# Optimization experiments

Hardware: AMD Instinct MI355X
Metric: run time of the kernel (lower is better)

The kernel has to match this reference:

```python
import jax, jax.numpy as jnp
import numpy as np

N_NODES = 10000
N_EDGES = 320000
NODE_F = 64
EDGE_F = 32
H = 256
L = 6
HEADS = 8
OUT = H // HEADS
N_GRAPHS = 16
NEG_SLOPE = 0.2  # PyG GATConv leaky_relu slope


def setup_inputs() -> dict:
    key = jax.random.key(0)
    ks = jax.random.split(key, 32)
    s = 0.05
    f32 = jnp.float32
    inp = {}
    inp["x"] = jax.random.normal(ks[0], (N_NODES, NODE_F), f32)
    inp["edge_index"] = jax.random.randint(ks[1], (2, N_EDGES), 0, N_NODES)
    inp["edge_attr"] = jax.random.normal(ks[2], (N_EDGES, EDGE_F), f32)
    inp["batch"] = jnp.sort(jax.random.randint(ks[3], (N_NODES,), 0, N_GRAPHS))
    # embeddings
    inp["node_w"] = jax.random.normal(ks[4], (H, NODE_F), f32) * s
    inp["node_b"] = jnp.zeros((H,), f32)
    inp["edge_emb_w"] = jax.random.normal(ks[5], (H, EDGE_F), f32) * s
    inp["edge_emb_b"] = jnp.zeros((H,), f32)
    # stacked GATConv params (shared lin for src/dst since in_channels is int)
    inp["lin_w"] = jax.random.normal(ks[6], (L, H, H), f32) * s
    inp["att_src"] = jax.random.normal(ks[7], (L, HEADS, OUT), f32) * s
    inp["att_dst"] = jax.random.normal(ks[8], (L, HEADS, OUT), f32) * s
    inp["att_edge"] = jax.random.normal(ks[9], (L, HEADS, OUT), f32) * s
    inp["lin_edge_w"] = jax.random.normal(ks[10], (L, H, H), f32) * s
    inp["conv_b"] = jnp.zeros((L, H), f32)
    inp["ln_g"] = jnp.ones((L, H), f32)
    inp["ln_b"] = jnp.zeros((L, H), f32)
    # MLP heads: Linear(2H->H), Linear(H->H/2), Linear(H/2->3)
    inp["pw1"] = jax.random.normal(ks[11], (H, 2 * H), f32) * s
    inp["pb1"] = jnp.zeros((H,), f32)
    inp["pw2"] = jax.random.normal(ks[12], (H // 2, H), f32) * s
    inp["pb2"] = jnp.zeros((H // 2,), f32)
    inp["pw3"] = jax.random.normal(ks[13], (3, H // 2), f32) * s
    inp["pb3"] = jnp.zeros((3,), f32)
    inp["mw1"] = jax.random.normal(ks[14], (H, 2 * H), f32) * s
    inp["mb1"] = jnp.zeros((H,), f32)
    inp["mw2"] = jax.random.normal(ks[15], (H // 2, H), f32) * s
    inp["mb2"] = jnp.zeros((H // 2,), f32)
    inp["mw3"] = jax.random.normal(ks[16], (3, H // 2), f32) * s
    inp["mb3"] = jnp.zeros((3,), f32)
    return inp


def _ln(x, g, b):
    mu = jnp.mean(x, -1, keepdims=True)
    var = jnp.mean(jnp.square(x - mu), -1, keepdims=True)
    return g * (x - mu) * jax.lax.rsqrt(var + 1e-5) + b


def _mlp(z, w1, b1, w2, b2, w3, b3):
    h = jax.nn.gelu(z @ w1.T + b1, approximate=False)
    h = jax.nn.gelu(h @ w2.T + b2, approximate=False)
    return jax.nn.sigmoid(h @ w3.T + b3)


def _gnn_forward(x, edge_attr, src, dst, batch,
                 node_w, node_b, edge_emb_w, edge_emb_b,
                 lin_w, att_src, att_dst, att_edge, lin_edge_w, conv_b,
                 ln_g, ln_b,
                 pw1, pb1, pw2, pb2, pw3, pb3,
                 mw1, mb1, mw2, mb2, mw3, mb3):
    h = x @ node_w.T + node_b                       # [N, H]
    ea = edge_attr @ edge_emb_w.T + edge_emb_b      # [E, H]
    # PyG add_self_loops(fill_value='mean'): loop attr = mean of incoming edge attrs
    cnt = jax.ops.segment_sum(jnp.ones((N_EDGES,), h.dtype), dst, N_NODES)
    loop_attr = jax.ops.segment_sum(ea, dst, N_NODES) / jnp.maximum(cnt, 1.0)[:, None]
    ea_full = jnp.concatenate([ea, loop_attr], 0)   # [E+N, H]
    loops = jnp.arange(N_NODES, dtype=src.dtype)
    src_f = jnp.concatenate([src, loops])
    dst_f = jnp.concatenate([dst, loops])
    for i in range(L):
        x_in = h
        xw = (h @ lin_w[i].T).reshape(N_NODES, HEADS, OUT)
        eap = (ea_full @ lin_edge_w[i].T).reshape(-1, HEADS, OUT)
        a_src = jnp.sum(xw * att_src[i], -1)        # [N, heads]
        a_dst = jnp.sum(xw * att_dst[i], -1)
        alpha = a_src[src_f] + a_dst[dst_f] + jnp.sum(eap * att_edge[i], -1)  # [E+N, heads]
        alpha = jnp.where(alpha > 0, alpha, NEG_SLOPE * alpha)
        amax = jax.ops.segment_max(alpha, dst_f, N_NODES)
        e = jnp.exp(alpha - amax[dst_f])
        denom = jax.ops.segment_sum(e, dst_f, N_NODES)
        w = e / (denom[dst_f] + 1e-16)
        msg = xw[src_f] * w[:, :, None]             # [E+N, heads, out]
        hi = jax.ops.segment_sum(msg, dst_f, N_NODES).reshape(N_NODES, H) + conv_b[i]
        hi = jax.nn.gelu(_ln(hi, ln_g[i], ln_b[i]), approximate=False)
        h = hi + x_in if i > 0 else hi
    sums = jax.ops.segment_sum(h, batch, N_GRAPHS)  # [G, H]
    ncnt = jax.ops.segment_sum(jnp.ones((N_NODES,), h.dtype), batch, N_GRAPHS)
    mean = sums / jnp.maximum(ncnt, 1.0)[:, None]
    xg = jnp.concatenate([mean, sums], 1)           # [G, 2H]
    params = _mlp(xg, pw1, pb1, pw2, pb2, pw3, pb3)
    metrics = _mlp(xg, mw1, mb1, mw2, mb2, mw3, mb3)
    return params, metrics


def reference(x, edge_index, edge_attr, batch,
              node_w, node_b, edge_emb_w, edge_emb_b,
              lin_w, att_src, att_dst, att_edge, lin_edge_w, conv_b,
              ln_g, ln_b,
              pw1, pb1, pw2, pb2, pw3, pb3,
              mw1, mb1, mw2, mb2, mw3, mb3):
    return _gnn_forward(x, edge_attr, edge_index[0], edge_index[1], batch,
                        node_w, node_b, edge_emb_w, edge_emb_b,
                        lin_w, att_src, att_dst, att_edge, lin_edge_w, conv_b,
                        ln_g, ln_b,
                        pw1, pb1, pw2, pb2, pw3, pb3,
                        mw1, mb1, mw2, mb2, mw3, mb3)
```

## Files before the change

### kernel.cpp

```cpp
#include <hip/hip_runtime.h>
#include <math.h>

#define NN 10000
#define NE 320000
#define NODE_F 64
#define EDGE_F 32
#define HDIM 256
#define HEADS 8
#define LAYERS 6
#define NG 16
#define NPB 2
#define NOUT 48
#define LOG2E 1.4426950408889634f

typedef __attribute__((ext_vector_type(8))) short short8;
typedef __attribute__((ext_vector_type(4))) float float4v;
typedef __attribute__((ext_vector_type(2))) float floatx2;

__global__ void count_kernel(const int* __restrict__ dst, int* __restrict__ cnt) {
    int e = blockIdx.x * 256 + threadIdx.x;
    if (e < NE) atomicAdd(&cnt[dst[e]], 1);
}

__global__ void scan_kernel(const int* __restrict__ cnt, int* __restrict__ row_ptr,
                            int* __restrict__ pos) {
    __shared__ int part[1024];
    int t = threadIdx.x;
    const int chunk = (NN + 1023) / 1024;
    int lo = t * chunk, hi = min(NN, lo + chunk);
    int s = 0;
    for (int i = lo; i < hi; ++i) s += cnt[i];
    part[t] = s;
    __syncthreads();
    for (int off = 1; off < 1024; off <<= 1) {
        int v = (t >= off) ? part[t - off] : 0;
        __syncthreads();
        part[t] += v;
        __syncthreads();
    }
    int base = (t == 0) ? 0 : part[t - 1];
    for (int i = lo; i < hi; ++i) {
        row_ptr[i] = base;
        pos[i] = base;
        base += cnt[i];
    }
    if (t == 1023) row_ptr[NN] = part[1023];
}

__device__ __forceinline__ ushort f2bf(float f) {
    union { float f; unsigned u; } v; v.f = f;
    unsigned u = v.u;
    return (ushort)((u + 0x7fffu + ((u >> 16) & 1u)) >> 16);
}
__device__ __forceinline__ float bf2f(ushort b) {
    union { unsigned u; float f; } v; v.u = ((unsigned)b) << 16; return v.f;
}

__global__ void scatter_kernel(const int* __restrict__ src, const int* __restrict__ dst,
                               const float* __restrict__ edge_attr,
                               int* __restrict__ pos, int* __restrict__ csr_src,
                               ushort* __restrict__ ea_bf) {
    int e = blockIdx.x * 256 + threadIdx.x;
    if (e >= NE) return;
    int d = dst[e];
    int idx = atomicAdd(&pos[d], 1);
    csr_src[idx] = src[e];
    const float4* p = (const float4*)(edge_attr + (size_t)e * EDGE_F);
    uint4* q = (uint4*)(ea_bf + (size_t)idx * EDGE_F);
    #pragma unroll
    for (int i = 0; i < 4; ++i) {
        float4 v0 = p[i * 2], v1 = p[i * 2 + 1];
        uint4 pk;
        pk.x = (unsigned)f2bf(v0.x) | ((unsigned)f2bf(v0.y) << 16);
        pk.y = (unsigned)f2bf(v0.z) | ((unsigned)f2bf(v0.w) << 16);
        pk.z = (unsigned)f2bf(v1.x) | ((unsigned)f2bf(v1.y) << 16);
        pk.w = (unsigned)f2bf(v1.z) | ((unsigned)f2bf(v1.w) << 16);
        q[i] = pk;
    }
}

__global__ __launch_bounds__(256) void prep_kernel(const float* __restrict__ att_edge,
                                                   const float* __restrict__ lin_edge_w,
                                                   const float* __restrict__ eew,
                                                   const float* __restrict__ eeb,
                                                   ushort* __restrict__ webbf,
                                                   float* __restrict__ bebuf) {
    int ih = blockIdx.x;
    int i = ih >> 3, h = ih & 7;
    __shared__ float vsh[HDIM];
    int t = threadIdx.x;
    float s = 0.f;
    const float* ae = att_edge + ih * 32;
    const float* lw = lin_edge_w + ((size_t)i * HDIM + h * 32) * HDIM + t;
    #pragma unroll
    for (int o = 0; o < 32; ++o) s += ae[o] * lw[(size_t)o * HDIM];
    vsh[t] = s;
    __syncthreads();
    if (t < EDGE_F) {
        float acc = 0.f;
        for (int k = 0; k < HDIM; ++k) acc += vsh[k] * eew[k * EDGE_F + t];
        webbf[ih * EDGE_F + t] = f2bf(acc * LOG2E);
    } else if (t == EDGE_F) {
        float acc = 0.f;
        for (int k = 0; k < HDIM; ++k) acc += vsh[k] * eeb[k];
        bebuf[ih] = acc * LOG2E;
    }
}

__global__ __launch_bounds__(256) void preE_kernel(const ushort* __restrict__ ea_bf,
                                                   const ushort* __restrict__ web,
                                                   const float* __restrict__ be,
                                                   ushort* __restrict__ preEb) {
    int wv = threadIdx.x >> 6, l = threadIdx.x & 63;
    int base = blockIdx.x * 64 + wv * 16;
    int m = l & 15, kq = (l >> 4) * 8;
    short8 afrag = *(const short8*)(ea_bf + (size_t)(base + m) * EDGE_F + kq);
    float4v zero = {0.f, 0.f, 0.f, 0.f};
    float4v acc[3];
    #pragma unroll
    for (int ct = 0; ct < 3; ++ct) {
        short8 bfrag = *(const short8*)(web + (size_t)(ct * 16 + m) * EDGE_F + kq);
        acc[ct] = __builtin_amdgcn_mfma_f32_16x16x32_bf16(afrag, bfrag, zero, 0, 0, 0);
    }
    #pragma unroll
    for (int ct = 0; ct < 3; ++ct) {
        int oc = ct * 16 + m;
        int li = oc >> 3, hh = oc & 7;
        float bv = be[oc];
        #pragma unroll
        for (int r = 0; r < 4; ++r) {
            int row = (l >> 4) * 4 + r;
            preEb[(size_t)li * NE * 8 + (size_t)(base + row) * 8 + hh] = f2bf(acc[ct][r] + bv);
        }
    }
}

__global__ __launch_bounds__(256) void preL_kernel(const ushort* __restrict__ preEb,
                                                   const int* __restrict__ row_ptr,
                                                   float* __restrict__ preL) {
    int g = threadIdx.x >> 5, c = threadIdx.x & 31;
    int n = blockIdx.x * 8 + g;
    int start = row_ptr[n], end = row_ptr[n + 1];
    int deg = end - start;
    float s[NOUT] = {};
    for (int idx = start + c; idx < end; idx += 32) {
        #pragma unroll
        for (int li = 0; li < LAYERS; ++li) {
            uint4 pk = *(const uint4*)(preEb + (size_t)li * NE * 8 + (size_t)idx * 8);
            s[li * 8 + 0] += bf2f((ushort)(pk.x & 0xffff));
            s[li * 8 + 1] += bf2f((ushort)(pk.x >> 16));
            s[li * 8 + 2] += bf2f((ushort)(pk.y & 0xffff));
            s[li * 8 + 3] += bf2f((ushort)(pk.y >> 16));
            s[li * 8 + 4] += bf2f((ushort)(pk.z & 0xffff));
            s[li * 8 + 5] += bf2f((ushort)(pk.z >> 16));
            s[li * 8 + 6] += bf2f((ushort)(pk.w & 0xffff));
            s[li * 8 + 7] += bf2f((ushort)(pk.w >> 16));
        }
    }
    #pragma unroll
    for (int off = 16; off >= 1; off >>= 1)
        #pragma unroll
        for (int h = 0; h < NOUT; ++h) s[h] += __shfl_xor(s[h], off, 32);
    if (c == 0) {
        float invd = deg > 0 ? 1.f / (float)deg : 0.f;
        for (int li = 0; li < LAYERS; ++li) {
            float4* dstp = (float4*)(preL + ((size_t)li * NN + n) * 8);
            dstp[0] = make_float4(s[li * 8 + 0] * invd, s[li * 8 + 1] * invd,
                                  s[li * 8 + 2] * invd, s[li * 8 + 3] * invd);
            dstp[1] = make_float4(s[li * 8 + 4] * invd, s[li * 8 + 5] * invd,
                                  s[li * 8 + 6] * invd, s[li * 8 + 7] * invd);
        }
    }
}

__global__ void tobf_all_kernel(const float* __restrict__ lin_w, const float* __restrict__ node_w,
                                const float* __restrict__ x, ushort* __restrict__ wbhi,
                                ushort* __restrict__ nwhi, ushort* __restrict__ xhi) {
    const int N1 = LAYERS * HDIM * HDIM;
    const int N2 = N1 + HDIM * NODE_F;
    const int N3 = N2 + NN * NODE_F;
    int i = blockIdx.x * 256 + threadIdx.x;
    if (i < N1) wbhi[i] = f2bf(lin_w[i]);
    else if (i < N2) nwhi[i - N1] = f2bf(node_w[i - N1]);
    else if (i < N3) xhi[i - N2] = f2bf(x[i - N2]);
}

__global__ __launch_bounds__(128) void gemm_bf1(const ushort* __restrict__ Ah,
                                                const ushort* __restrict__ Bh,
                                                const float* __restrict__ bias,
                                                float* __restrict__ C,
                                                ushort* __restrict__ Chi,
                                                unsigned char* __restrict__ Cf8,
                                                const float* __restrict__ att_s,
                                                const float* __restrict__ att_d,
                                                float* __restrict__ a_src,
                                                float* __restrict__ a_dst,
                                                int N, int K, int J) {
    __shared__ ushort sAh[64][40], sBh[64][40];
    int nb = blockIdx.y * 64, jb = blockIdx.x * 64;
    int t = threadIdx.x, w = t >> 6, l = t & 63;
    int srow = t >> 1, sq = (t & 1) * 16;
    int fr = l & 15, fq = (l >> 4) * 8;
    float4v acc[2][4] = {};
    for (int kt = 0; kt < K; kt += 32) {
        int gr = nb + srow;
        short8 a0 = {0,0,0,0,0,0,0,0}, a1 = {0,0,0,0,0,0,0,0};
        if (gr < N) {
            const short8* pa = (const short8*)(Ah + (size_t)gr * K + kt + sq);
            a0 = pa[0]; a1 = pa[1];
        }
        *(short8*)&sAh[srow][sq] = a0; *(short8*)&sAh[srow][sq + 8] = a1;
        const short8* pb = (const short8*)(Bh + (size_t)(jb + srow) * K + kt + sq);
        short8 b0 = pb[0], b1 = pb[1];
        *(short8*)&sBh[srow][sq] = b0; *(short8*)&sBh[srow][sq + 8] = b1;
        __syncthreads();
        short8 bh[4];
        #pragma unroll
        for (int nt = 0; nt < 4; ++nt)
            bh[nt] = *(const short8*)&sBh[nt * 16 + fr][fq];
        #pragma unroll
        for (int mt = 0; mt < 2; ++mt) {
            short8 ah = *(const short8*)&sAh[w * 32 + mt * 16 + fr][fq];
            #pragma unroll
            for (int nt = 0; nt < 4; ++nt)
                acc[mt][nt] = __builtin_amdgcn_mfma_f32_16x16x32_bf16(ah, bh[nt], acc[mt][nt], 0, 0, 0);
        }
        __syncthreads();
    }
    #pragma unroll
    for (int mt = 0; mt < 2; ++mt) {
        #pragma unroll
        for (int nt = 0; nt < 4; ++nt) {
            int col = jb + nt * 16 + fr;
            float bv = bias ? bias[col] : 0.f;
            #pragma unroll
            for (int r = 0; r < 4; ++r) {
                int row = nb + w * 32 + mt * 16 + (l >> 4) * 4 + r;
                if (row < N) {
                    float v = acc[mt][nt][r] + bv;
                    if (C) C[(size_t)row * J + col] = v;
                    if (Chi) Chi[(size_t)row * J + col] = f2bf(v);
                    if (Cf8) {
                        int pk8 = __builtin_amdgcn_cvt_pk_fp8_f32(v, v, 0, false);
                        Cf8[(size_t)row * J + col] = (unsigned char)(pk8 & 0xff);
                    }
                }
            }
        }
    }
    if (att_s) {
        int head0 = jb >> 5;
        float cs[4], cd[4];
        #pragma unroll
        for (int nt = 0; nt < 4; ++nt) {
            cs[nt] = att_s[jb + nt * 16 + fr] * LOG2E;
            cd[nt] = att_d[jb + nt * 16 + fr] * LOG2E;
        }
        #pragma unroll
        for (int mt = 0; mt < 2; ++mt) {
            #pragma unroll
            for (int r = 0; r < 4; ++r) {
                float s0 = acc[mt][0][r] * cs[0] + acc[mt][1][r] * cs[1];
                float s1 = acc[mt][2][r] * cs[2] + acc[mt][3][r] * cs[3];
                float d0 = acc[mt][0][r] * cd[0] + acc[mt][1][r] * cd[1];
                float d1 = acc[mt][2][r] * cd[2] + acc[mt][3][r] * cd[3];
                #pragma unroll
                for (int off = 8; off >= 1; off >>= 1) {
                    s0 += __shfl_xor(s0, off, 16);
                    s1 += __shfl_xor(s1, off, 16);
                    d0 += __shfl_xor(d0, off, 16);
                    d1 += __shfl_xor(d1, off, 16);
                }
                if (fr == 0) {
                    int row = nb + w * 32 + mt * 16 + (l >> 4) * 4 + r;
                    if (row < N) {
                        a_src[row * 8 + head0]     = s0;
                        a_src[row * 8 + head0 + 1] = s1;
                        a_dst[row * 8 + head0]     = d0;
                        a_dst[row * 8 + head0 + 1] = d1;
                    }
                }
            }
        }
    }
}

__device__ __forceinline__ float gelu_exact(float x) {
    return 0.5f * x * (1.f + erff(x * 0.70710678118654752f));
}

__global__ __launch_bounds__(64 * NPB) void node_kernel(const unsigned char* __restrict__ xwf8,
                                                  const ushort* __restrict__ pb,
                                                  const float* __restrict__ preL,
                                                  const float* __restrict__ a_src,
                                                  const float* __restrict__ a_dst,
                                                  const int* __restrict__ row_ptr,
                                                  const int* __restrict__ csr_src,
                                                  const float* __restrict__ h_prev,
                                                  float* __restrict__ h_next,
                                                  ushort* __restrict__ hhi,
                                                  const float* __restrict__ cb,
                                                  const float* __restrict__ lg,
                                                  const float* __restrict__ lb, int first) {
    int wv = threadIdx.x >> 6, l = threadIdx.x & 63;
    int n = blockIdx.x * NPB + wv;
    int start = row_ptr[n], end = row_ptr[n + 1];
    int hc = l >> 3;
    float adnh = a_dst[n * 8 + hc];
    const unsigned char* xb = xwf8 + 4 * l;

    float den, acc[4];
    {
        float al = a_src[n * 8 + hc] + adnh + preL[n * 8 + hc];
        al = fminf(fmaxf(al, 0.2f * al), 57.7f);
        float wself = exp2f(al);
        den = wself;
        unsigned gs = *(const unsigned*)(xb + (size_t)n * HDIM);
        floatx2 lo = __builtin_amdgcn_cvt_pk_f32_fp8(gs, false);
        floatx2 hi = __builtin_amdgcn_cvt_pk_f32_fp8(gs, true);
        acc[0] = wself * lo.x;
        acc[1] = wself * lo.y;
        acc[2] = wself * hi.x;
        acc[3] = wself * hi.y;
    }
    int idx = start;
    for (; idx + 8 <= end; idx += 8) {
        int sn[8];
        unsigned g[8];
        float p[8], a[8], w8[8];
        #pragma unroll
        for (int j = 0; j < 8; ++j) sn[j] = csr_src[idx + j];
        #pragma unroll
        for (int j = 0; j < 8; ++j) g[j] = *(const unsigned*)(xb + (size_t)sn[j] * HDIM);
        #pragma unroll
        for (int j = 0; j < 8; ++j) p[j] = bf2f(pb[(size_t)(idx + j) * 8 + hc]);
        #pragma unroll
        for (int j = 0; j < 8; ++j) a[j] = a_src[(size_t)sn[j] * 8 + hc] + adnh + p[j];
        #pragma unroll
        for (int j = 0; j < 8; ++j)
            w8[j] = exp2f(fminf(fmaxf(a[j], 0.2f * a[j]), 57.7f));
        #pragma unroll
        for (int j = 0; j < 8; ++j) {
            floatx2 lo = __builtin_amdgcn_cvt_pk_f32_fp8(g[j], false);
            floatx2 hi = __builtin_amdgcn_cvt_pk_f32_fp8(g[j], true);
            den += w8[j];
            acc[0] += w8[j] * lo.x;
            acc[1] += w8[j] * lo.y;
            acc[2] += w8[j] * hi.x;
            acc[3] += w8[j] * hi.y;
        }
    }
    for (; idx < end; ++idx) {
        int sn = csr_src[idx];
        unsigned g = *(const unsigned*)(xb + (size_t)sn * HDIM);
        float a = a_src[(size_t)sn * 8 + hc] + adnh + bf2f(pb[(size_t)idx * 8 + hc]);
        float wt = exp2f(fminf(fmaxf(a, 0.2f * a), 57.7f));
        floatx2 lo = __builtin_amdgcn_cvt_pk_f32_fp8(g, false);
        floatx2 hi = __builtin_amdgcn_cvt_pk_f32_fp8(g, true);
        den += wt;
        acc[0] += wt * lo.x;
        acc[1] += wt * lo.y;
        acc[2] += wt * hi.x;
        acc[3] += wt * hi.y;
    }
    float4 cb4 = *(const float4*)(cb + 4 * l);
    float invh = 1.f / (den + 1e-16f);
    acc[0] = acc[0] * invh + cb4.x;
    acc[1] = acc[1] * invh + cb4.y;
    acc[2] = acc[2] * invh + cb4.z;
    acc[3] = acc[3] * invh + cb4.w;

    float part = acc[0] + acc[1] + acc[2] + acc[3];
    #pragma unroll
    for (int off = 32; off >= 1; off >>= 1) part += __shfl_xor(part, off, 64);
    float mu = part * (1.f / 256.f);
    float p2 = 0.f;
    #pragma unroll
    for (int j = 0; j < 4; ++j) {
        float d = acc[j] - mu;
        p2 += d * d;
    }
    #pragma unroll
    for (int off = 32; off >= 1; off >>= 1) p2 += __shfl_xor(p2, off, 64);
    float rstd = rsqrtf(p2 * (1.f / 256.f) + 1e-5f);

    float4 lg4 = *(const float4*)(lg + 4 * l);
    float4 lb4 = *(const float4*)(lb + 4 * l);
    float o4[4];
    float lgv[4] = {lg4.x, lg4.y, lg4.z, lg4.w};
    float lbv[4] = {lb4.x, lb4.y, lb4.z, lb4.w};
    float4 hp = make_float4(0.f, 0.f, 0.f, 0.f);
    if (!first) hp = *(const float4*)(h_prev + (size_t)n * HDIM + 4 * l);
    float hpv[4] = {hp.x, hp.y, hp.z, hp.w};
    #pragma unroll
    for (int j = 0; j < 4; ++j) {
        float y = (acc[j] - mu) * rstd * lgv[j] + lbv[j];
        o4[j] = gelu_exact(y) + hpv[j];
    }
    *(float4*)(h_next + (size_t)n * HDIM + 4 * l) = make_float4(o4[0], o4[1], o4[2], o4[3]);
    if (hhi) {
        uint2 ph;
        ph.x = (unsigned)f2bf(o4[0]) | ((unsigned)f2bf(o4[1]) << 16);
        ph.y = (unsigned)f2bf(o4[2]) | ((unsigned)f2bf(o4[3]) << 16);
        *(uint2*)(hhi + (size_t)n * HDIM + 4 * l) = ph;
    }
}

__global__ __launch_bounds__(256) void graph_sum_kernel(const float* __restrict__ h,
                                                        const int* __restrict__ batch,
                                                        float* __restrict__ sums) {
    int t = threadIdx.x;
    int n0 = blockIdx.x * 64;
    int n1 = min(NN, n0 + 64);
    float acc = 0.f;
    int cur = batch[n0];
    for (int n = n0; n < n1; ++n) {
        int b = batch[n];
        if (b != cur) {
            atomicAdd(&sums[cur * HDIM + t], acc);
            acc = 0.f;
            cur = b;
        }
        acc += h[(size_t)n * HDIM + t];
    }
    atomicAdd(&sums[cur * HDIM + t], acc);
}

__device__ __forceinline__ int lower_bound_dev(const int* a, int n, int v) {
    int lo = 0, hi = n;
    while (lo < hi) {
        int mid = (lo + hi) >> 1;
        if (a[mid] < v) lo = mid + 1; else hi = mid;
    }
    return lo;
}

__global__ __launch_bounds__(256) void mlp_kernel(const float* __restrict__ sums,
                                                  const int* __restrict__ batch,
                                                  const float* __restrict__ pw1,
                                                  const float* __restrict__ pb1,
                                                  const float* __restrict__ pw2,
                                                  const float* __restrict__ pb2,
                                                  const float* __restrict__ pw3,
                                                  const float* __restrict__ pb3,
                                                  const float* __restrict__ mw1,
                                                  const float* __restrict__ mb1,
                                                  const float* __restrict__ mw2,
                                                  const float* __restrict__ mb2,
                                                  const float* __restrict__ mw3,
                                                  const float* __restrict__ mb3,
                                                  float* __restrict__ out) {
    int g = blockIdx.x, which = blockIdx.y;
    const float* w1 = which ? mw1 : pw1; const float* b1 = which ? mb1 : pb1;
    const float* w2 = which ? mw2 : pw2; const float* b2 = which ? mb2 : pb2;
    const float* w3 = which ? mw3 : pw3; const float* b3 = which ? mb3 : pb3;
    __shared__ float xg[512];
    __shared__ float h1[256];
    __shared__ float h2[128];
    __shared__ float cinv_s;
    int t = threadIdx.x;
    if (t == 0) {
        int s0 = lower_bound_dev(batch, NN, g), s1 = lower_bound_dev(batch, NN, g + 1);
        cinv_s = 1.f / fmaxf((float)(s1 - s0), 1.f);
    }
    __syncthreads();
    float sv = sums[g * HDIM + t];
    xg[t] = sv * cinv_s;
    xg[256 + t] = sv;
    __syncthreads();
    {
        const float* wr = w1 + (size_t)t * 512;
        float acc = 0.f;
        #pragma unroll 8
        for (int k = 0; k < 512; k += 4) {
            float4 wv = *(const float4*)(wr + k);
            acc += wv.x * xg[k] + wv.y * xg[k + 1] + wv.z * xg[k + 2] + wv.w * xg[k + 3];
        }
        h1[t] = gelu_exact(acc + b1[t]);
    }
    __syncthreads();
    {
        int row = t >> 1, hf = t & 1;
        const float* wr = w2 + (size_t)row * 256 + hf * 128;
        const float* hx = h1 + hf * 128;
        float acc = 0.f;
        #pragma unroll 8
        for (int k = 0; k < 128; k += 4) {
            float4 wv = *(const float4*)(wr + k);
            acc += wv.x * hx[k] + wv.y * hx[k + 1] + wv.z * hx[k + 2] + wv.w * hx[k + 3];
        }
        acc += __shfl_xor(acc, 1, 64);
        if (hf == 0) h2[row] = gelu_exact(acc + b2[row]);
    }
    __syncthreads();
    if (t < 64) {
        float v0 = h2[t], v1 = h2[64 + t];
        #pragma unroll
        for (int o = 0; o < 3; ++o) {
            float p = w3[o * 128 + t] * v0 + w3[o * 128 + 64 + t] * v1;
            #pragma unroll
            for (int off = 32; off >= 1; off >>= 1) p += __shfl_xor(p, off, 64);
            if (t == 0) out[which * (NG * 3) + g * 3 + o] = 1.f / (1.f + expf(-(p + b3[o])));
        }
    }
}

extern "C" void kernel_launch(void* const* d_in, const int* in_sizes, int n_in, void* d_out,
                              int out_size, void* d_ws, size_t ws_size, hipStream_t stream) {
    const float* x         = (const float*)d_in[0];
    const int*   ei        = (const int*)d_in[1];
    const int*   src       = ei;
    const int*   dst       = ei + NE;
    const float* edge_attr = (const float*)d_in[2];
    const int*   batch     = (const int*)d_in[3];
    const float* node_w    = (const float*)d_in[4];
    const float* node_b    = (const float*)d_in[5];
    const float* eew       = (const float*)d_in[6];
    const float* eeb       = (const float*)d_in[7];
    const float* lin_w     = (const float*)d_in[8];
    const float* att_src   = (const float*)d_in[9];
    const float* att_dst   = (const float*)d_in[10];
    const float* att_edge  = (const float*)d_in[11];
    const float* lin_edge_w= (const float*)d_in[12];
    const float* conv_b    = (const float*)d_in[13];
    const float* ln_g      = (const float*)d_in[14];
    const float* ln_b      = (const float*)d_in[15];
    const float* pw1 = (const float*)d_in[16]; const float* pb1 = (const float*)d_in[17];
    const float* pw2 = (const float*)d_in[18]; const float* pb2 = (const float*)d_in[19];
    const float* pw3 = (const float*)d_in[20]; const float* pb3 = (const float*)d_in[21];
    const float* mw1 = (const float*)d_in[22]; const float* mb1 = (const float*)d_in[23];
    const float* mw2 = (const float*)d_in[24]; const float* mb2 = (const float*)d_in[25];
    const float* mw3 = (const float*)d_in[26]; const float* mb3 = (const float*)d_in[27];
    float* out = (float*)d_out;

    float* wsf = (float*)d_ws;
    float* hA        = wsf; wsf += (size_t)NN * HDIM;
    float* hB        = wsf; wsf += (size_t)NN * HDIM;
    float* preL      = wsf; wsf += (size_t)LAYERS * NN * 8;
    float* a_src     = wsf; wsf += (size_t)NN * HEADS;
    float* a_dst     = wsf; wsf += (size_t)NN * HEADS;
    float* bebuf     = wsf; wsf += 64;
    ushort* ubuf = (ushort*)wsf;
    ushort* ea_bf = ubuf; ubuf += (size_t)NE * EDGE_F;
    ushort* preEb = ubuf; ubuf += (size_t)NE * NOUT;
    ushort* webbf = ubuf; ubuf += (size_t)NOUT * EDGE_F;
    ushort* hhi  = ubuf; ubuf += (size_t)NN * HDIM;
    unsigned char* xwf8 = (unsigned char*)ubuf; ubuf += (size_t)NN * HDIM / 2;
    ushort* wbhi = ubuf; ubuf += (size_t)LAYERS * HDIM * HDIM;
    ushort* xhi  = ubuf; ubuf += (size_t)NN * NODE_F;
    ushort* nwhi = ubuf; ubuf += (size_t)HDIM * NODE_F;
    int* ibuf    = (int*)ubuf;
    int* cnt     = ibuf; ibuf += NN + 16;
    float* sums  = (float*)ibuf; ibuf += NG * HDIM;
    int* row_ptr = ibuf; ibuf += NN + 16;
    int* pos     = ibuf; ibuf += NN + 16;
    int* csr_src = ibuf; ibuf += NE;

    hipMemsetAsync(cnt, 0, (NN + 16 + NG * HDIM) * sizeof(int), stream);
    count_kernel<<<(NE + 255) / 256, 256, 0, stream>>>(dst, cnt);
    scan_kernel<<<1, 1024, 0, stream>>>(cnt, row_ptr, pos);
    scatter_kernel<<<(NE + 255) / 256, 256, 0, stream>>>(src, dst, edge_attr, pos, csr_src,
                                                         ea_bf);

    prep_kernel<<<LAYERS * HEADS, 256, 0, stream>>>(att_edge, lin_edge_w, eew, eeb, webbf, bebuf);
    preE_kernel<<<NE / 64, 256, 0, stream>>>(ea_bf, webbf, bebuf, preEb);
    preL_kernel<<<NN / 8, 256, 0, stream>>>(preEb, row_ptr, preL);

    {
        const int total = LAYERS * HDIM * HDIM + HDIM * NODE_F + NN * NODE_F;
        tobf_all_kernel<<<(total + 255) / 256, 256, 0, stream>>>(lin_w, node_w, x,
                                                                 wbhi, nwhi, xhi);
    }

    {
        dim3 grid(HDIM / 64, (NN + 63) / 64);
        gemm_bf1<<<grid, 128, 0, stream>>>(xhi, nwhi, node_b, nullptr, hhi, nullptr,
                                           nullptr, nullptr, nullptr, nullptr,
                                           NN, NODE_F, HDIM);
    }

    float* cur = hA;
    float* nxt = hB;
    for (int i = 0; i < LAYERS; ++i) {
        dim3 grid(HDIM / 64, (NN + 63) / 64);
        gemm_bf1<<<grid, 128, 0, stream>>>(hhi, wbhi + (size_t)i * HDIM * HDIM, nullptr,
                                           nullptr, nullptr, xwf8,
                                           att_src + i * HEADS * 32, att_dst + i * HEADS * 32,
                                           a_src, a_dst, NN, HDIM, HDIM);
        node_kernel<<<NN / NPB, 64 * NPB, 0, stream>>>(
            xwf8, preEb + (size_t)i * NE * 8, preL + (size_t)i * NN * 8, a_src, a_dst,
            row_ptr, csr_src, cur, nxt, (i == LAYERS - 1) ? nullptr : hhi,
            conv_b + i * HDIM, ln_g + i * HDIM, ln_b + i * HDIM, i == 0 ? 1 : 0);
        float* tmp = cur; cur = nxt; nxt = tmp;
    }

    graph_sum_kernel<<<(NN + 63) / 64, 256, 0, stream>>>(cur, batch, sums);
    {
        dim3 gm(NG, 2);
        mlp_kernel<<<gm, 256, 0, stream>>>(sums, batch, pw1, pb1, pw2, pb2, pw3, pb3,
                                           mw1, mb1, mw2, mb2, mw3, mb3, out);
    }
}
```

Before: 542.5 us.

## Fuse edge scatter into preE GEMM, wave-shuffle scan, and lane-parallel attention weights

Merges the CSR scatter kernel into the edge-attention projection kernel. Edge attributes are now converted to bf16 in registers and the results are written straight to CSR order through shuffled atomic slots, so the bf16 edge-attribute buffer round trip goes away. The single-block scan now uses wave shuffles instead of a shared-memory Hillis-Steele loop with many barriers. In the node kernel, each of 8 lanes per head computes one edge's attention weight, which is then broadcast with shuffles, removing 8x redundant a_src loads and exp computations per lane. Scattered preEb writes may coalesce less well than the earlier sequential writes.

```diff
diff --git a/kernel.cpp b/kernel.cpp
--- a/kernel.cpp
+++ b/kernel.cpp
@@ -24,27 +24,50 @@
 
 __global__ void scan_kernel(const int* __restrict__ cnt, int* __restrict__ row_ptr,
                             int* __restrict__ pos) {
-    __shared__ int part[1024];
+    __shared__ int wsum[16];
+    __shared__ int woff[16];
     int t = threadIdx.x;
-    const int chunk = (NN + 1023) / 1024;
-    int lo = t * chunk, hi = min(NN, lo + chunk);
+    int lane = t & 63, wid = t >> 6;
+    const int chunk = 10;
+    int lo = t * chunk;
+    int loc[10];
     int s = 0;
-    for (int i = lo; i < hi; ++i) s += cnt[i];
-    part[t] = s;
+    #pragma unroll
+    for (int k = 0; k < 10; ++k) {
+        int i = lo + k;
+        int v = (i < NN) ? cnt[i] : 0;
+        loc[k] = v;
+        s += v;
+    }
+    int inc = s;
+    #pragma unroll
+    for (int off = 1; off < 64; off <<= 1) {
+        int v = __shfl_up(inc, off, 64);
+        if (lane >= off) inc += v;
+    }
+    if (lane == 63) wsum[wid] = inc;
     __syncthreads();
-    for (int off = 1; off < 1024; off <<= 1) {
-        int v = (t >= off) ? part[t - off] : 0;
-        __syncthreads();
-        part[t] += v;
-        __syncthreads();
-    }
-    int base = (t == 0) ? 0 : part[t - 1];
-    for (int i = lo; i < hi; ++i) {
-        row_ptr[i] = base;
-        pos[i] = base;
-        base += cnt[i];
-    }
-    if (t == 1023) row_ptr[NN] = part[1023];
+    if (t < 16) {
+        int inc2 = wsum[t];
+        #pragma unroll
+        for (int off = 1; off < 16; off <<= 1) {
+            int u = __shfl_up(inc2, off, 16);
+            if (t >= off) inc2 += u;
+        }
+        woff[t] = inc2;
+    }
+    __syncthreads();
+    int base = inc - s + (wid ? woff[wid - 1] : 0);
+    #pragma unroll
+    for (int k = 0; k < 10; ++k) {
+        int i = lo + k;
+        if (i < NN) {
+            row_ptr[i] = base;
+            pos[i] = base;
+            base += loc[k];
+        }
+    }
+    if (t == 1023) row_ptr[NN] = woff[15];
 }
 
 __device__ __forceinline__ ushort f2bf(float f) {
@@ -54,29 +77,6 @@
 }
 __device__ __forceinline__ float bf2f(ushort b) {
     union { unsigned u; float f; } v; v.u = ((unsigned)b) << 16; return v.f;
-}
-
-__global__ void scatter_kernel(const int* __restrict__ src, const int* __restrict__ dst,
-                               const float* __restrict__ edge_attr,
-                               int* __restrict__ pos, int* __restrict__ csr_src,
-                               ushort* __restrict__ ea_bf) {
-    int e = blockIdx.x * 256 + threadIdx.x;
-    if (e >= NE) return;
-    int d = dst[e];
-    int idx = atomicAdd(&pos[d], 1);
-    csr_src[idx] = src[e];
-    const float4* p = (const float4*)(edge_attr + (size_t)e * EDGE_F);
-    uint4* q = (uint4*)(ea_bf + (size_t)idx * EDGE_F);
-    #pragma unroll
-    for (int i = 0; i < 4; ++i) {
-        float4 v0 = p[i * 2], v1 = p[i * 2 + 1];
-        uint4 pk;
-        pk.x = (unsigned)f2bf(v0.x) | ((unsigned)f2bf(v0.y) << 16);
-        pk.y = (unsigned)f2bf(v0.z) | ((unsigned)f2bf(v0.w) << 16);
-        pk.z = (unsigned)f2bf(v1.x) | ((unsigned)f2bf(v1.y) << 16);
-        pk.w = (unsigned)f2bf(v1.z) | ((unsigned)f2bf(v1.w) << 16);
-        q[i] = pk;
-    }
 }
 
 __global__ __launch_bounds__(256) void prep_kernel(const float* __restrict__ att_edge,
@@ -107,14 +107,32 @@
     }
 }
 
-__global__ __launch_bounds__(256) void preE_kernel(const ushort* __restrict__ ea_bf,
-                                                   const ushort* __restrict__ web,
-                                                   const float* __restrict__ be,
-                                                   ushort* __restrict__ preEb) {
+__global__ __launch_bounds__(256) void scatterE_kernel(const int* __restrict__ src,
+                                                       const int* __restrict__ dst,
+                                                       const float* __restrict__ edge_attr,
+                                                       int* __restrict__ pos,
+                                                       int* __restrict__ csr_src,
+                                                       const ushort* __restrict__ web,
+                                                       const float* __restrict__ be,
+                                                       ushort* __restrict__ preEb) {
     int wv = threadIdx.x >> 6, l = threadIdx.x & 63;
     int base = blockIdx.x * 64 + wv * 16;
     int m = l & 15, kq = (l >> 4) * 8;
-    short8 afrag = *(const short8*)(ea_bf + (size_t)(base + m) * EDGE_F + kq);
+    int idxl = 0;
+    if (l < 16) {
+        int e = base + l;
+        int d = dst[e];
+        idxl = atomicAdd(&pos[d], 1);
+        csr_src[idxl] = src[e];
+    }
+    const float* ar = edge_attr + (size_t)(base + m) * EDGE_F + kq;
+    float4 a0 = *(const float4*)(ar);
+    float4 a1 = *(const float4*)(ar + 4);
+    short8 afrag;
+    afrag[0] = (short)f2bf(a0.x); afrag[1] = (short)f2bf(a0.y);
+    afrag[2] = (short)f2bf(a0.z); afrag[3] = (short)f2bf(a0.w);
+    afrag[4] = (short)f2bf(a1.x); afrag[5] = (short)f2bf(a1.y);
+    afrag[6] = (short)f2bf(a1.z); afrag[7] = (short)f2bf(a1.w);
     float4v zero = {0.f, 0.f, 0.f, 0.f};
     float4v acc[3];
     #pragma unroll
@@ -130,7 +148,8 @@
         #pragma unroll
         for (int r = 0; r < 4; ++r) {
             int row = (l >> 4) * 4 + r;
-            preEb[(size_t)li * NE * 8 + (size_t)(base + row) * 8 + hh] = f2bf(acc[ct][r] + bv);
+            int ridx = __shfl(idxl, row, 64);
+            preEb[(size_t)li * NE * 8 + (size_t)ridx * 8 + hh] = f2bf(acc[ct][r] + bv);
         }
     }
 }
@@ -306,6 +325,8 @@
     int n = blockIdx.x * NPB + wv;
     int start = row_ptr[n], end = row_ptr[n + 1];
     int hc = l >> 3;
+    int hc8 = l & 56;
+    int jj = l & 7;
     float adnh = a_dst[n * 8 + hc];
     const unsigned char* xb = xwf8 + 4 * l;
 
@@ -326,28 +347,25 @@
     int idx = start;
     for (; idx + 8 <= end; idx += 8) {
         int sn[8];
+        #pragma unroll
+        for (int j = 0; j < 8; ++j) sn[j] = csr_src[idx + j];
+        int sn_t = csr_src[idx + jj];
+        float p_t = bf2f(pb[(size_t)(idx + jj) * 8 + hc]);
+        float a_t = a_src[(size_t)sn_t * 8 + hc] + adnh + p_t;
+        float w_t = exp2f(fminf(fmaxf(a_t, 0.2f * a_t), 57.7f));
         unsigned g[8];
-        float p[8], a[8], w8[8];
-        #pragma unroll
-        for (int j = 0; j < 8; ++j) sn[j] = csr_src[idx + j];
         #pragma unroll
         for (int j = 0; j < 8; ++j) g[j] = *(const unsigned*)(xb + (size_t)sn[j] * HDIM);
         #pragma unroll
-        for (int j = 0; j < 8; ++j) p[j] = bf2f(pb[(size_t)(idx + j) * 8 + hc]);
-        #pragma unroll
-        for (int j = 0; j < 8; ++j) a[j] = a_src[(size_t)sn[j] * 8 + hc] + adnh + p[j];
-        #pragma unroll
-        for (int j = 0; j < 8; ++j)
-            w8[j] = exp2f(fminf(fmaxf(a[j], 0.2f * a[j]), 57.7f));
-        #pragma unroll
         for (int j = 0; j < 8; ++j) {
+            float wj = __shfl(w_t, hc8 + j, 64);
             floatx2 lo = __builtin_amdgcn_cvt_pk_f32_fp8(g[j], false);
             floatx2 hi = __builtin_amdgcn_cvt_pk_f32_fp8(g[j], true);
-            den += w8[j];
-            acc[0] += w8[j] * lo.x;
-            acc[1] += w8[j] * lo.y;
-            acc[2] += w8[j] * hi.x;
-            acc[3] += w8[j] * hi.y;
+            den += wj;
+            acc[0] += wj * lo.x;
+            acc[1] += wj * lo.y;
+            acc[2] += wj * hi.x;
+            acc[3] += wj * hi.y;
         }
     }
     for (; idx < end; ++idx) {
@@ -541,7 +559,6 @@
     float* a_dst     = wsf; wsf += (size_t)NN * HEADS;
     float* bebuf     = wsf; wsf += 64;
     ushort* ubuf = (ushort*)wsf;
-    ushort* ea_bf = ubuf; ubuf += (size_t)NE * EDGE_F;
     ushort* preEb = ubuf; ubuf += (size_t)NE * NOUT;
     ushort* webbf = ubuf; ubuf += (size_t)NOUT * EDGE_F;
     ushort* hhi  = ubuf; ubuf += (size_t)NN * HDIM;
@@ -559,11 +576,10 @@
     hipMemsetAsync(cnt, 0, (NN + 16 + NG * HDIM) * sizeof(int), stream);
     count_kernel<<<(NE + 255) / 256, 256, 0, stream>>>(dst, cnt);
     scan_kernel<<<1, 1024, 0, stream>>>(cnt, row_ptr, pos);
-    scatter_kernel<<<(NE + 255) / 256, 256, 0, stream>>>(src, dst, edge_attr, pos, csr_src,
-                                                         ea_bf);
 
     prep_kernel<<<LAYERS * HEADS, 256, 0, stream>>>(att_edge, lin_edge_w, eew, eeb, webbf, bebuf);
-    preE_kernel<<<NE / 64, 256, 0, stream>>>(ea_bf, webbf, bebuf, preEb);
+    scatterE_kernel<<<NE / 64, 256, 0, stream>>>(src, dst, edge_attr, pos, csr_src,
+                                                 webbf, bebuf, preEb);
     preL_kernel<<<NN / 8, 256, 0, stream>>>(preEb, row_ptr, preL);
 
     {
```

Result: faster. 524.4 us (-3.3%).
